# Optimization experiments

Measured on AMD Instinct MI355X. Metric: run time of the kernel, lower is better.

The kernel has to match this reference:

```python
import jax, jax.numpy as jnp
import numpy as np

D = 128  # input_size


def setup_inputs() -> dict:
    key = jax.random.key(0)
    k0, k1, k2, k3 = jax.random.split(key, 4)
    B, S = 4, 4096
    inp = jax.random.normal(k0, (B, S, D), dtype=jnp.float32)
    # nn.Linear weights, stored as [out, in] like torch
    Wq = jax.random.normal(k1, (D, D), dtype=jnp.float32) * (1.0 / np.sqrt(D))
    Wk = jax.random.normal(k2, (D, D), dtype=jnp.float32) * (1.0 / np.sqrt(D))
    Wv = jax.random.normal(k3, (D, D), dtype=jnp.float32) * (1.0 / np.sqrt(D))
    return {"input": inp, "Wq": Wq, "Wk": Wk, "Wv": Wv}


def reference(input, Wq, Wk, Wv):
    # torch Linear: y = x @ W.T
    q = jnp.einsum('bsd,ed->bse', input, Wq)
    k = jnp.einsum('bsd,ed->bse', input, Wk)
    v = jnp.einsum('bsd,ed->bse', input, Wv)
    # NOTE: module divides by input_size (D), not sqrt(D)
    scores = jnp.einsum('bqe,bke->bqk', q, k) / D  # [B,S,S]
    attn = jax.nn.softmax(scores, axis=2)
    return jnp.einsum('bqk,bke->bqe', attn, v)
```

## Files before the change

kernel.cpp:

```cpp
#include <hip/hip_runtime.h>
#include <stdint.h>

#define B_ 4
#define S_ 4096
#define D_ 128
#define KVB 32
#define NT (S_ / KVB)
#define NR (B_ * S_)

typedef __bf16 bf16;
typedef __bf16 bf16x8 __attribute__((ext_vector_type(8)));
typedef float f32x4 __attribute__((ext_vector_type(4)));

#define QB_OFF  0
#define KB_OFF  (QB_OFF + B_*S_*D_*2)
#define VTB_OFF (KB_OFF + B_*S_*D_*2)
#define ACC_OFF (VTB_OFF + B_*S_*D_*2)

#define GLOAD_LDS16(g, l)                                                    \
  __builtin_amdgcn_global_load_lds(                                          \
      (const __attribute__((address_space(1))) void*)(g),                    \
      (__attribute__((address_space(3))) void*)(l), 16, 0, 0)

__global__ __launch_bounds__(256) void proj_kernel(const float* __restrict__ x,
    const float* __restrict__ wq, const float* __restrict__ wk,
    const float* __restrict__ wv, bf16* __restrict__ qb, bf16* __restrict__ kb,
    bf16* __restrict__ vtb) {
  __shared__ bf16 ct[64][136];
  __shared__ __align__(16) bf16 wl[128 * 128];
  const int tid  = threadIdx.x;
  const int wave = tid >> 6, lane = tid & 63;
  const int lrow = lane & 15, g = lane >> 4;
  const int m = blockIdx.y;
  const float* w = (m == 0) ? wq : (m == 1 ? wk : wv);
  const int row0b = blockIdx.x * 64;
  const int row0  = row0b + wave * 16;

#pragma unroll
  for (int it = 0; it < 8; ++it) {
    int chv = it * 256 + tid;
    int row = chv >> 4, pos = chv & 15;
    const float4* wp = (const float4*)(w + (size_t)chv * 8);
    float4 w0 = wp[0], w1 = wp[1];
    bf16x8 v;
    v[0]=(bf16)w0.x; v[1]=(bf16)w0.y; v[2]=(bf16)w0.z; v[3]=(bf16)w0.w;
    v[4]=(bf16)w1.x; v[5]=(bf16)w1.y; v[6]=(bf16)w1.z; v[7]=(bf16)w1.w;
    *(bf16x8*)(&wl[row * 128 + ((pos ^ (row & 15)) * 8)]) = v;
  }

  bf16x8 af[4];
  {
    const float* xp = x + (size_t)(row0 + lrow) * D_ + g * 8;
#pragma unroll
    for (int ks = 0; ks < 4; ++ks) {
      const float4* p4 = (const float4*)(xp + ks * 32);
      float4 a0 = p4[0], a1 = p4[1];
      bf16x8 v;
      v[0]=(bf16)a0.x; v[1]=(bf16)a0.y; v[2]=(bf16)a0.z; v[3]=(bf16)a0.w;
      v[4]=(bf16)a1.x; v[5]=(bf16)a1.y; v[6]=(bf16)a1.z; v[7]=(bf16)a1.w;
      af[ks] = v;
    }
  }
  __syncthreads();

  f32x4 acc[8];
#pragma unroll
  for (int c = 0; c < 8; ++c) acc[c] = (f32x4){0.f, 0.f, 0.f, 0.f};
#pragma unroll
  for (int c = 0; c < 8; ++c) {
#pragma unroll
    for (int ks = 0; ks < 4; ++ks) {
      bf16x8 bf = *(const bf16x8*)(
          &wl[(c * 16 + lrow) * 128 + (((ks * 4 + g) ^ lrow) * 8)]);
      acc[c] = __builtin_amdgcn_mfma_f32_16x16x32_bf16(af[ks], bf, acc[c], 0, 0, 0);
    }
  }
#pragma unroll
  for (int c = 0; c < 8; ++c)
#pragma unroll
    for (int r = 0; r < 4; ++r)
      ct[wave * 16 + g * 4 + r][c * 16 + lrow] = (bf16)acc[c][r];
  __syncthreads();

  if (m < 2) {
    bf16* ob = (m == 0) ? qb : kb;
#pragma unroll
    for (int it = 0; it < 4; ++it) {
      int chunk = it * 256 + tid;
      int row = chunk >> 4, pos = chunk & 15;
      *(bf16x8*)(ob + (size_t)(row0b + row) * D_ + pos * 8) =
          *(const bf16x8*)(&ct[row][pos * 8]);
    }
  } else {
    const int b = row0b / S_;
    const int sb = row0b & (S_ - 1);
#pragma unroll
    for (int it = 0; it < 4; ++it) {
      int ci = it * 256 + tid;
      int e = ci >> 3, hc = ci & 7;
      int h = hc >> 2, gg = hc & 3;
      bf16x8 v;
#pragma unroll
      for (int j = 0; j < 8; ++j)
        v[j] = ct[h * 32 + ((j >> 2) * 16 + gg * 4 + (j & 3))][e];
      *(bf16x8*)(vtb + (size_t)(b * D_ + e) * S_ + sb + h * 32 + gg * 8) = v;
    }
  }
}

__global__ __launch_bounds__(256, 2) void attn_kernel(const bf16* __restrict__ qb,
    const bf16* __restrict__ kb, const bf16* __restrict__ vtb,
    float* __restrict__ out, bf16* __restrict__ accP, float* __restrict__ lP,
    int ns) {
  __shared__ __align__(16) bf16 Kt[3][KVB * 128];
  __shared__ __align__(16) bf16 Vt[3][128 * KVB];

  const int tid  = threadIdx.x;
  const int wave = tid >> 6, lane = tid & 63;
  const int lrow = lane & 15, g = lane >> 4;

  const int nwg = gridDim.x;
  int gid = blockIdx.x;
  if ((nwg & 7) == 0) gid = (gid & 7) * (nwg >> 3) + (gid >> 3);
  const int qp  = gid & 127;
  const int seg = gid >> 7;
  const int b   = qp >> 5;
  const int q0  = (qp & 31) * 128 + wave * 32;

  const int base = NT / ns, ext = NT % ns;
  const int cnt  = base + (seg < ext);
  const int t0   = seg * base + (seg < ext ? seg : ext);
  const int tend = t0 + cnt;

  const float SC = 1.4426950408889634f / 128.0f;
  const float MC = 1.4426950408889634f;

  int koff[2], voff[2], kd[2];
#pragma unroll
  for (int it = 0; it < 2; ++it) {
    int ci = (wave * 2 + it) * 64 + lane;
    int krow = ci >> 4, kch = (ci & 15) ^ (krow & 15);
    koff[it] = krow * D_ + kch * 8;
    int q = ci >> 3, tt = (ci & 7) ^ (q & 7);
    int d = 2 * q + (tt >> 2), vch = tt & 3;
    voff[it] = d * S_ + vch * 8;
    kd[it] = (wave * 2 + it) * 512;
  }
  const int vrb = ((lrow >> 1) * 8 + ((((lrow & 1) * 4 + g)) ^ ((lrow >> 1) & 7))) * 8;

  bf16x8 qf[2][4];
#pragma unroll
  for (int a = 0; a < 2; ++a) {
    const bf16* qp_ = qb + (size_t)(b * S_ + q0 + a * 16 + lrow) * D_ + g * 8;
#pragma unroll
    for (int ks = 0; ks < 4; ++ks) qf[a][ks] = *(const bf16x8*)(qp_ + ks * 32);
  }

  f32x4 acc[2][8];
#pragma unroll
  for (int a = 0; a < 2; ++a)
#pragma unroll
    for (int c = 0; c < 8; ++c) acc[a][c] = (f32x4){0.f, 0.f, 0.f, 0.f};
  float l_r[2] = {0.f, 0.f};

  const bf16* kbase = kb + (size_t)b * S_ * D_;
  const bf16* vbase = vtb + (size_t)b * D_ * S_;

#define STAGE(tt, buf)                                                       \
  { const bf16* kp_ = kbase + (size_t)(tt) * KVB * D_;                       \
    const bf16* vp_ = vbase + (tt) * KVB;                                    \
    GLOAD_LDS16(kp_ + koff[0], &Kt[buf][kd[0]]);                             \
    GLOAD_LDS16(kp_ + koff[1], &Kt[buf][kd[1]]);                             \
    GLOAD_LDS16(vp_ + voff[0], &Vt[buf][kd[0]]);                             \
    GLOAD_LDS16(vp_ + voff[1], &Vt[buf][kd[1]]); }

  STAGE(t0, 0);
  if (t0 + 1 < tend) STAGE(t0 + 1, 1);

  int bcur = 0;
  for (int t = t0; t < tend; ++t) {
    if (t + 1 < tend) {
      asm volatile("s_waitcnt vmcnt(4)\n\ts_barrier" ::: "memory");
    } else {
      asm volatile("s_waitcnt vmcnt(0)\n\ts_barrier" ::: "memory");
    }
    int bnxt = bcur + 2; if (bnxt >= 3) bnxt -= 3;
    if (t + 2 < tend) STAGE(t + 2, bnxt);

    f32x4 s[2][2];
#pragma unroll
    for (int a = 0; a < 2; ++a)
#pragma unroll
      for (int ti = 0; ti < 2; ++ti) s[a][ti] = (f32x4){0.f, 0.f, 0.f, 0.f};
    __builtin_amdgcn_s_setprio(1);
#pragma unroll
    for (int ti = 0; ti < 2; ++ti) {
#pragma unroll
      for (int ks = 0; ks < 4; ++ks) {
        const int row = ti * 16 + lrow;
        bf16x8 kf = *(const bf16x8*)(
            &Kt[bcur][row * 128 + (((ks * 4 + g) ^ lrow) * 8)]);
        s[0][ti] = __builtin_amdgcn_mfma_f32_16x16x32_bf16(kf, qf[0][ks], s[0][ti], 0, 0, 0);
        s[1][ti] = __builtin_amdgcn_mfma_f32_16x16x32_bf16(kf, qf[1][ks], s[1][ti], 0, 0, 0);
      }
    }
    __builtin_amdgcn_s_setprio(0);

    float ts[2] = {0.f, 0.f};
#pragma unroll
    for (int a = 0; a < 2; ++a)
#pragma unroll
      for (int ti = 0; ti < 2; ++ti)
#pragma unroll
        for (int r = 0; r < 4; ++r) {
          float e = __builtin_amdgcn_exp2f(__builtin_fmaf(s[a][ti][r], SC, -MC));
          s[a][ti][r] = e;
          ts[a] += e;
        }
    l_r[0] += ts[0];
    l_r[1] += ts[1];

    bf16x8 pa[2];
#pragma unroll
    for (int a = 0; a < 2; ++a) {
      bf16x8 v;
#pragma unroll
      for (int r = 0; r < 4; ++r) {
        v[r]     = (bf16)s[a][0][r];
        v[4 + r] = (bf16)s[a][1][r];
      }
      pa[a] = v;
    }

    __builtin_amdgcn_s_setprio(1);
#pragma unroll
    for (int c = 0; c < 8; ++c) {
      bf16x8 vf = *(const bf16x8*)(&Vt[bcur][vrb + c * 512]);
      acc[0][c] = __builtin_amdgcn_mfma_f32_16x16x32_bf16(pa[0], vf, acc[0][c], 0, 0, 0);
      acc[1][c] = __builtin_amdgcn_mfma_f32_16x16x32_bf16(pa[1], vf, acc[1][c], 0, 0, 0);
    }
    __builtin_amdgcn_s_setprio(0);

    bcur = (bcur + 1 == 3) ? 0 : bcur + 1;
  }
#undef STAGE

#pragma unroll
  for (int a = 0; a < 2; ++a) {
    l_r[a] += __shfl_xor(l_r[a], 16);
    l_r[a] += __shfl_xor(l_r[a], 32);
  }

  if (ns == 1) {
#pragma unroll
    for (int a = 0; a < 2; ++a) {
      float linv[4];
#pragma unroll
      for (int r = 0; r < 4; ++r) linv[r] = 1.0f / __shfl(l_r[a], g * 4 + r);
#pragma unroll
      for (int c = 0; c < 8; ++c)
#pragma unroll
        for (int r = 0; r < 4; ++r) {
          int row = q0 + a * 16 + g * 4 + r;
          out[(size_t)(b * S_ + row) * D_ + c * 16 + lrow] = acc[a][c][r] * linv[r];
        }
    }
  } else {
#pragma unroll
    for (int a = 0; a < 2; ++a) {
#pragma unroll
      for (int c = 0; c < 8; ++c)
#pragma unroll
        for (int r = 0; r < 4; ++r) {
          int row = b * S_ + q0 + a * 16 + g * 4 + r;
          accP[(((size_t)seg * NR + row) << 7) + c * 16 + lrow] = (bf16)acc[a][c][r];
        }
      if (g == 0) {
        int row = b * S_ + q0 + a * 16 + lrow;
        lP[(size_t)seg * NR + row] = l_r[a];
      }
    }
  }
}

__global__ __launch_bounds__(256) void combine_kernel(const bf16* __restrict__ accP,
    const float* __restrict__ lP, float* __restrict__ out, int ns) {
  const int t = blockIdx.x * 256 + threadIdx.x;
  const int row = t >> 4, d = (t & 15) * 8;
  float L = 0.f;
  float o[8] = {0.f, 0.f, 0.f, 0.f, 0.f, 0.f, 0.f, 0.f};
  for (int i = 0; i < ns; ++i) {
    L += lP[(size_t)i * NR + row];
    bf16x8 a = *(const bf16x8*)(&accP[(((size_t)i * NR + row) << 7) + d]);
#pragma unroll
    for (int j = 0; j < 8; ++j) o[j] += (float)a[j];
  }
  float inv = 1.0f / L;
  float4 o0 = make_float4(o[0]*inv, o[1]*inv, o[2]*inv, o[3]*inv);
  float4 o1 = make_float4(o[4]*inv, o[5]*inv, o[6]*inv, o[7]*inv);
  float* op = &out[(size_t)row * 128 + d];
  *(float4*)op = o0;
  *(float4*)(op + 4) = o1;
}

extern "C" void kernel_launch(void* const* d_in, const int* in_sizes, int n_in,
                              void* d_out, int out_size, void* d_ws, size_t ws_size,
                              hipStream_t stream) {
  const float* x  = (const float*)d_in[0];
  const float* wq = (const float*)d_in[1];
  const float* wk = (const float*)d_in[2];
  const float* wv = (const float*)d_in[3];
  float* out = (float*)d_out;
  char* ws = (char*)d_ws;
  bf16* qb  = (bf16*)(ws + QB_OFF);
  bf16* kb  = (bf16*)(ws + KB_OFF);
  bf16* vtb = (bf16*)(ws + VTB_OFF);

  const size_t acc1 = (size_t)NR * D_ * 2;
  const size_t l1   = (size_t)NR * 4;
  int ns = 6;
  if (ws_size < ACC_OFF + 6 * (acc1 + l1)) ns = 4;
  if (ws_size < ACC_OFF + 4 * (acc1 + l1)) ns = 2;
  if (ws_size < ACC_OFF + 2 * (acc1 + l1)) ns = 1;
  bf16* accP = (bf16*)(ws + ACC_OFF);
  float* lp  = (float*)(ws + ACC_OFF + (size_t)ns * acc1);

  hipLaunchKernelGGL(proj_kernel, dim3(256, 3), dim3(256), 0, stream,
                     x, wq, wk, wv, qb, kb, vtb);
  hipLaunchKernelGGL(attn_kernel, dim3(128 * ns), dim3(256), 0, stream,
                     qb, kb, vtb, out, accP, lp, ns);
  if (ns > 1)
    hipLaunchKernelGGL(combine_kernel, dim3(NR / 16), dim3(256), 0, stream,
                       accP, lp, out, ns);
}
```

Measured before the change: 59.40 us.

## Double KV tile to 64, double-buffer, and fold softmax scale into Q projection

Raises the attention KV tile from 32 to 64 rows and goes from triple to double buffering, so each barrier covers twice the MFMA work. The V tile layout and swizzle are reworked to match. The 1/128·log2e scale is now applied to Q in the projection kernel, and the constant offset before exp2 is dropped, which removes an FMA per score. The split count drops from 6 to 4 segments. The cost is weaker load/compute overlap, since every iteration now waits on vmcnt(0), and fewer workgroups in the attention grid.

```diff
diff --git a/kernel.cpp b/kernel.cpp
--- a/kernel.cpp
+++ b/kernel.cpp
@@ -4,7 +4,7 @@
 #define B_ 4
 #define S_ 4096
 #define D_ 128
-#define KVB 32
+#define KVB 64
 #define NT (S_ / KVB)
 #define NR (B_ * S_)
 
@@ -35,6 +35,7 @@
   const float* w = (m == 0) ? wq : (m == 1 ? wk : wv);
   const int row0b = blockIdx.x * 64;
   const int row0  = row0b + wave * 16;
+  const float SC = 1.4426950408889634f / 128.0f;
 
 #pragma unroll
   for (int it = 0; it < 8; ++it) {
@@ -75,11 +76,12 @@
       acc[c] = __builtin_amdgcn_mfma_f32_16x16x32_bf16(af[ks], bf, acc[c], 0, 0, 0);
     }
   }
+  const float osc = (m == 0) ? SC : 1.0f;
 #pragma unroll
   for (int c = 0; c < 8; ++c)
 #pragma unroll
     for (int r = 0; r < 4; ++r)
-      ct[wave * 16 + g * 4 + r][c * 16 + lrow] = (bf16)acc[c][r];
+      ct[wave * 16 + g * 4 + r][c * 16 + lrow] = (bf16)(acc[c][r] * osc);
   __syncthreads();
 
   if (m < 2) {
@@ -112,8 +114,8 @@
     const bf16* __restrict__ kb, const bf16* __restrict__ vtb,
     float* __restrict__ out, bf16* __restrict__ accP, float* __restrict__ lP,
     int ns) {
-  __shared__ __align__(16) bf16 Kt[3][KVB * 128];
-  __shared__ __align__(16) bf16 Vt[3][128 * KVB];
+  __shared__ __align__(16) bf16 Kt[2][KVB * 128];
+  __shared__ __align__(16) bf16 Vt[2][128 * KVB];
 
   const int tid  = threadIdx.x;
   const int wave = tid >> 6, lane = tid & 63;
@@ -132,21 +134,16 @@
   const int t0   = seg * base + (seg < ext ? seg : ext);
   const int tend = t0 + cnt;
 
-  const float SC = 1.4426950408889634f / 128.0f;
-  const float MC = 1.4426950408889634f;
-
-  int koff[2], voff[2], kd[2];
-#pragma unroll
-  for (int it = 0; it < 2; ++it) {
-    int ci = (wave * 2 + it) * 64 + lane;
+  int koff[4], voff[4], kd[4];
+#pragma unroll
+  for (int it = 0; it < 4; ++it) {
+    int ci = (wave * 4 + it) * 64 + lane;
     int krow = ci >> 4, kch = (ci & 15) ^ (krow & 15);
     koff[it] = krow * D_ + kch * 8;
-    int q = ci >> 3, tt = (ci & 7) ^ (q & 7);
-    int d = 2 * q + (tt >> 2), vch = tt & 3;
+    int d = ci >> 3, vch = (ci & 7) ^ (d & 7);
     voff[it] = d * S_ + vch * 8;
-    kd[it] = (wave * 2 + it) * 512;
-  }
-  const int vrb = ((lrow >> 1) * 8 + ((((lrow & 1) * 4 + g)) ^ ((lrow >> 1) & 7))) * 8;
+    kd[it] = (wave * 4 + it) * 512;
+  }
 
   bf16x8 qf[2][4];
 #pragma unroll
@@ -171,30 +168,28 @@
     const bf16* vp_ = vbase + (tt) * KVB;                                    \
     GLOAD_LDS16(kp_ + koff[0], &Kt[buf][kd[0]]);                             \
     GLOAD_LDS16(kp_ + koff[1], &Kt[buf][kd[1]]);                             \
+    GLOAD_LDS16(kp_ + koff[2], &Kt[buf][kd[2]]);                             \
+    GLOAD_LDS16(kp_ + koff[3], &Kt[buf][kd[3]]);                             \
     GLOAD_LDS16(vp_ + voff[0], &Vt[buf][kd[0]]);                             \
-    GLOAD_LDS16(vp_ + voff[1], &Vt[buf][kd[1]]); }
+    GLOAD_LDS16(vp_ + voff[1], &Vt[buf][kd[1]]);                             \
+    GLOAD_LDS16(vp_ + voff[2], &Vt[buf][kd[2]]);                             \
+    GLOAD_LDS16(vp_ + voff[3], &Vt[buf][kd[3]]); }
 
   STAGE(t0, 0);
-  if (t0 + 1 < tend) STAGE(t0 + 1, 1);
-
-  int bcur = 0;
+
   for (int t = t0; t < tend; ++t) {
-    if (t + 1 < tend) {
-      asm volatile("s_waitcnt vmcnt(4)\n\ts_barrier" ::: "memory");
-    } else {
-      asm volatile("s_waitcnt vmcnt(0)\n\ts_barrier" ::: "memory");
-    }
-    int bnxt = bcur + 2; if (bnxt >= 3) bnxt -= 3;
-    if (t + 2 < tend) STAGE(t + 2, bnxt);
-
-    f32x4 s[2][2];
+    const int bcur = (t - t0) & 1;
+    asm volatile("s_waitcnt vmcnt(0)\n\ts_barrier" ::: "memory");
+    if (t + 1 < tend) STAGE(t + 1, bcur ^ 1);
+
+    f32x4 s[2][4];
 #pragma unroll
     for (int a = 0; a < 2; ++a)
 #pragma unroll
-      for (int ti = 0; ti < 2; ++ti) s[a][ti] = (f32x4){0.f, 0.f, 0.f, 0.f};
+      for (int ti = 0; ti < 4; ++ti) s[a][ti] = (f32x4){0.f, 0.f, 0.f, 0.f};
     __builtin_amdgcn_s_setprio(1);
 #pragma unroll
-    for (int ti = 0; ti < 2; ++ti) {
+    for (int ti = 0; ti < 4; ++ti) {
 #pragma unroll
       for (int ks = 0; ks < 4; ++ks) {
         const int row = ti * 16 + lrow;
@@ -210,38 +205,43 @@
 #pragma unroll
     for (int a = 0; a < 2; ++a)
 #pragma unroll
-      for (int ti = 0; ti < 2; ++ti)
+      for (int ti = 0; ti < 4; ++ti)
 #pragma unroll
         for (int r = 0; r < 4; ++r) {
-          float e = __builtin_amdgcn_exp2f(__builtin_fmaf(s[a][ti][r], SC, -MC));
+          float e = __builtin_amdgcn_exp2f(s[a][ti][r]);
           s[a][ti][r] = e;
           ts[a] += e;
         }
     l_r[0] += ts[0];
     l_r[1] += ts[1];
 
-    bf16x8 pa[2];
-#pragma unroll
-    for (int a = 0; a < 2; ++a) {
-      bf16x8 v;
-#pragma unroll
-      for (int r = 0; r < 4; ++r) {
-        v[r]     = (bf16)s[a][0][r];
-        v[4 + r] = (bf16)s[a][1][r];
+    bf16x8 pa[2][2];
+#pragma unroll
+    for (int a = 0; a < 2; ++a)
+#pragma unroll
+      for (int bb = 0; bb < 2; ++bb) {
+        bf16x8 v;
+#pragma unroll
+        for (int r = 0; r < 4; ++r) {
+          v[r]     = (bf16)s[a][2 * bb][r];
+          v[4 + r] = (bf16)s[a][2 * bb + 1][r];
+        }
+        pa[a][bb] = v;
       }
-      pa[a] = v;
-    }
 
     __builtin_amdgcn_s_setprio(1);
 #pragma unroll
     for (int c = 0; c < 8; ++c) {
-      bf16x8 vf = *(const bf16x8*)(&Vt[bcur][vrb + c * 512]);
-      acc[0][c] = __builtin_amdgcn_mfma_f32_16x16x32_bf16(pa[0], vf, acc[0][c], 0, 0, 0);
-      acc[1][c] = __builtin_amdgcn_mfma_f32_16x16x32_bf16(pa[1], vf, acc[1][c], 0, 0, 0);
+      const int d = c * 16 + lrow;
+#pragma unroll
+      for (int bb = 0; bb < 2; ++bb) {
+        bf16x8 vf = *(const bf16x8*)(
+            &Vt[bcur][d * KVB + (((bb * 4 + g) ^ (d & 7)) * 8)]);
+        acc[0][c] = __builtin_amdgcn_mfma_f32_16x16x32_bf16(pa[0][bb], vf, acc[0][c], 0, 0, 0);
+        acc[1][c] = __builtin_amdgcn_mfma_f32_16x16x32_bf16(pa[1][bb], vf, acc[1][c], 0, 0, 0);
+      }
     }
     __builtin_amdgcn_s_setprio(0);
-
-    bcur = (bcur + 1 == 3) ? 0 : bcur + 1;
   }
 #undef STAGE
 
@@ -318,8 +318,7 @@
 
   const size_t acc1 = (size_t)NR * D_ * 2;
   const size_t l1   = (size_t)NR * 4;
-  int ns = 6;
-  if (ws_size < ACC_OFF + 6 * (acc1 + l1)) ns = 4;
+  int ns = 4;
   if (ws_size < ACC_OFF + 4 * (acc1 + l1)) ns = 2;
   if (ws_size < ACC_OFF + 2 * (acc1 + l1)) ns = 1;
   bf16* accP = (bf16*)(ws + ACC_OFF);
```

New measurement: 56.12 us. 5.5% less time.
